# Optimization experiments

Hardware: AMD Instinct MI355X
Metric: run time of the kernel (lower is better)

Reference implementation:

```python
import jax, jax.numpy as jnp
import numpy as np

WH = WW = 7          # window size
N_TOK = WH * WW      # 49 tokens per window
HEADS = 8
HEAD_DIM = 32
DIM = HEADS * HEAD_DIM  # 256
NW = 64              # windows per image (56x56 / 7x7)
BW = 64 * NW         # batch_images * windows = 4096


def _rel_pos_index(wh, ww):
    # Swin-style relative position index, flattened to (N*N,)
    coords = np.stack(np.meshgrid(np.arange(wh), np.arange(ww), indexing='ij'))  # (2, wh, ww)
    coords = coords.reshape(2, -1)                                               # (2, N)
    rel = coords[:, :, None] - coords[:, None, :]                                # (2, N, N)
    rel = rel.transpose(1, 2, 0).astype(np.int64)                                # (N, N, 2)
    rel[:, :, 0] += wh - 1
    rel[:, :, 1] += ww - 1
    rel[:, :, 0] *= 2 * ww - 1
    return jnp.asarray(rel.sum(-1).reshape(-1))                                  # (N*N,)

_REL_IDX = _rel_pos_index(WH, WW)


def setup_inputs() -> dict:
    key = jax.random.key(0)
    ks = jax.random.split(key, 5)
    x = jax.random.normal(ks[0], (BW, N_TOK, DIM), dtype=jnp.float32)
    mask = jnp.zeros((1, NW, 1, N_TOK, N_TOK), dtype=jnp.float32)
    w_qkv = jax.random.normal(ks[1], (DIM, 3 * HEADS * HEAD_DIM), dtype=jnp.float32) * 0.02
    b_qkv = jnp.zeros((3 * HEADS * HEAD_DIM,), dtype=jnp.float32)
    rel_table = jax.random.normal(ks[2], ((2 * WH - 1) * (2 * WW - 1), HEADS), dtype=jnp.float32) * 0.02
    w_out = jax.random.normal(ks[3], (HEADS * HEAD_DIM, DIM), dtype=jnp.float32) * 0.02
    b_out = jnp.zeros((DIM,), dtype=jnp.float32)
    return {"x": x, "mask": mask, "w_qkv": w_qkv, "b_qkv": b_qkv,
            "rel_table": rel_table, "w_out": w_out, "b_out": b_out}


def reference(x, mask, w_qkv, b_qkv, rel_table, w_out, b_out):
    bw, n, d = x.shape
    # QKV projection then split per original Rearrange:
    # 'b n (qkv h hd) -> qkv b h n hd'
    qkv = (x @ w_qkv + b_qkv).reshape(bw, n, 3, HEADS, HEAD_DIM)
    qkv = qkv.transpose(2, 0, 3, 1, 4)  # (3, bw, h, n, hd)
    q, k, v = qkv[0], qkv[1], qkv[2]
    # NOTE: original computes einsum('bnid,bnjd->bnij', k, q): a[i,j] = k_i . q_j
    a = jnp.einsum('bhid,bhjd->bhij', k, q) / jnp.sqrt(jnp.asarray(HEAD_DIM, x.dtype))
    # relative position bias: table gather then '(i j) h -> h i j'
    bias = rel_table[_REL_IDX].reshape(n, n, HEADS).transpose(2, 0, 1)  # (h, n, n)
    a = a + bias
    # mask add: '(b nW) h i j -> b nW h i j', + mask, back
    nw = mask.shape[1]
    a = a.reshape(bw // nw, nw, HEADS, n, n) + mask
    a = a.reshape(bw, HEADS, n, n)
    a = jax.nn.softmax(a, axis=-1)
    y = jnp.einsum('bhij,bhjd->bhid', a, v)        # (bw, h, n, hd)
    y = y.transpose(0, 2, 1, 3).reshape(bw, n, HEADS * HEAD_DIM)
    return y @ w_out + b_out
```

## Files before the change

### kernel.cpp

```cpp
#include <hip/hip_runtime.h>

typedef __attribute__((ext_vector_type(8))) short short8;
typedef __attribute__((ext_vector_type(4))) float f32x4;
typedef unsigned short u16;

#define NTOK 49
#define NBLK 4096

#define XF  0
#define QKP 16384
#define VTF 49152
#define MKF 65536
#define BQ  73728
#define BO  75264
#define POOL 75776

#define WS_WQT 0
#define WS_WOT 393216
#define WS_BIAS 524288

__device__ __forceinline__ u16 f2bf(float f) {
  unsigned u = __float_as_uint(f);
  return (u16)((u + 0x7fffu + ((u >> 16) & 1u)) >> 16);
}
__device__ __forceinline__ unsigned packbf(float a, float b) {
  return (unsigned)f2bf(a) | ((unsigned)f2bf(b) << 16);
}

__global__ void prep_kernel(const float* __restrict__ w_qkv,
                            const float* __restrict__ w_out,
                            const float* __restrict__ rel,
                            u16* __restrict__ wqTf,
                            u16* __restrict__ woTf,
                            float* __restrict__ biasf) {
  const int stride = gridDim.x * blockDim.x;
  const int gid = blockIdx.x * blockDim.x + threadIdx.x;
  for (int e = gid; e < 48 * 8 * 64 * 8; e += stride) {
    int eL = e & 7, ln = (e >> 3) & 63, ks = (e >> 9) & 7, ctg = e >> 12;
    int k = ks * 32 + (ln >> 4) * 8 + eL;
    int c = ctg * 16 + (ln & 15);
    wqTf[e] = f2bf(w_qkv[k * 768 + c]);
  }
  for (int e = gid; e < 16 * 8 * 64 * 8; e += stride) {
    int eL = e & 7, ln = (e >> 3) & 63, ks = (e >> 9) & 7, ctg = e >> 12;
    int k = ks * 32 + (ln >> 4) * 8 + eL;
    int c = ctg * 16 + (ln & 15);
    woTf[e] = f2bf(w_out[k * 256 + c]);
  }
  for (int e = gid; e < 8 * 16 * 64 * 4; e += stride) {
    int rg = e & 3, ln = (e >> 2) & 63, t = (e >> 8) & 15, hh = e >> 12;
    int i = (t >> 2) * 16 + (ln & 15);
    int j = (t & 3) * 16 + (ln >> 4) * 4 + rg;
    float v;
    if (j >= NTOK) v = -1e30f;
    else if (i >= NTOK) v = 0.f;
    else {
      int dh = i / 7 - j / 7 + 6;
      int dw = i % 7 - j % 7 + 6;
      v = rel[(dh * 13 + dw) * 8 + hh];
    }
    biasf[e] = v;
  }
}

__global__ void __launch_bounds__(1024, 4) winattn_mfma(
    const float* __restrict__ x,
    const float* __restrict__ mask,
    const float* __restrict__ b_qkv,
    const float* __restrict__ b_out,
    const u16* __restrict__ wqTf,
    const u16* __restrict__ woTf,
    const float* __restrict__ biasf,
    float* __restrict__ out)
{
  __shared__ u16 pool[POOL];
  const int b = blockIdx.x, tid = threadIdx.x;
  const int lane = tid & 63, lo = lane & 15, hi = lane >> 4;
  const int w = tid >> 6;
  const int h = w & 7;
  const int it0 = (w >> 3) * 2;
  const f32x4 zf = {0.f, 0.f, 0.f, 0.f};
  float* mkf = (float*)(pool + MKF);
  float* bq  = (float*)(pool + BQ);
  float* bo  = (float*)(pool + BO);

  {
    const float4* xg = (const float4*)(x + (size_t)b * (NTOK * 256));
    for (int e = tid; e < 49 * 64; e += 1024) {
      float4 v = xg[e];
      int r = e >> 6, c4 = (e & 63) << 2;
      int addr = (((r >> 4) * 8 + (c4 >> 5)) * 64 + ((c4 >> 3) & 3) * 16 + (r & 15)) * 8 + (c4 & 7);
      *(uint2*)&pool[XF + addr] = make_uint2(packbf(v.x, v.y), packbf(v.z, v.w));
    }
    if (tid < 15 * 64) {
      int e = tid;
      int r = 49 + (e >> 6), c4 = (e & 63) << 2;
      int addr = (((r >> 4) * 8 + (c4 >> 5)) * 64 + ((c4 >> 3) & 3) * 16 + (r & 15)) * 8 + (c4 & 7);
      *(uint2*)&pool[XF + addr] = make_uint2(0u, 0u);
    }
    const float* mrow = mask + (size_t)(b & 63) * (NTOK * NTOK);
    for (int e = tid; e < 4096; e += 1024) {
      int rg = e & 3, l = (e >> 2) & 63, t = e >> 8;
      int i = (t >> 2) * 16 + (l & 15);
      int j = (t & 3) * 16 + (l >> 4) * 4 + rg;
      mkf[e] = (i < NTOK && j < NTOK) ? mrow[i * NTOK + j] : 0.f;
    }
    if (tid < 768) bq[tid] = b_qkv[tid];
    if (tid < 256) bo[tid] = b_out[tid];
  }
  __syncthreads();

  {
    f32x4 acc[3][4];
    #pragma unroll
    for (int ct = 0; ct < 3; ++ct)
      #pragma unroll
      for (int rt = 0; rt < 4; ++rt) acc[ct][rt] = zf;
    #pragma unroll
    for (int ks = 0; ks < 8; ++ks) {
      short8 bx[4];
      #pragma unroll
      for (int rt = 0; rt < 4; ++rt)
        bx[rt] = *(const short8*)&pool[XF + ((rt * 8 + ks) * 64 + lane) * 8];
      #pragma unroll
      for (int ct = 0; ct < 3; ++ct) {
        short8 af = *(const short8*)&wqTf[((size_t)((3 * w + ct) * 8 + ks) * 64 + lane) * 8];
        #pragma unroll
        for (int rt = 0; rt < 4; ++rt)
          acc[ct][rt] = __builtin_amdgcn_mfma_f32_16x16x32_bf16(af, bx[rt], acc[ct][rt], 0, 0, 0);
      }
    }
    #pragma unroll
    for (int ct = 0; ct < 3; ++ct) {
      const int ctg = 3 * w + ct;
      const int head2 = (ctg & 15) >> 1;
      f32x4 bias = *(const f32x4*)&bq[ctg * 16 + hi * 4];
      #pragma unroll
      for (int rt = 0; rt < 4; ++rt) {
        f32x4 v = acc[ct][rt] + bias;
        if (ctg < 32) {
          int base = QKP + head2 * 4096 + (ctg >= 16 ? 2048 : 0);
          int hi2 = (ctg & 1) * 2 + (hi >> 1);
          int eb = (hi & 1) * 4;
          *(uint2*)&pool[base + (rt * 64 + hi2 * 16 + lo) * 8 + eb] =
              make_uint2(packbf(v[0], v[1]), packbf(v[2], v[3]));
        } else {
          int dblk = ctg & 1;
          int ks2 = rt >> 1;
          int hi2 = (rt & 1) * 2 + (lo >> 3);
          int e2 = lo & 7;
          int vb = VTF + head2 * 2048 + ((dblk * 2 + ks2) * 64 + hi2 * 16) * 8 + e2;
          pool[vb + (hi * 4 + 0) * 8] = f2bf(v[0]);
          pool[vb + (hi * 4 + 1) * 8] = f2bf(v[1]);
          pool[vb + (hi * 4 + 2) * 8] = f2bf(v[2]);
          pool[vb + (hi * 4 + 3) * 8] = f2bf(v[3]);
        }
      }
    }
  }
  __syncthreads();

  float rs0 = 0.f, rs1 = 0.f;
  unsigned pkp[4][2][2];
  {
    short8 ka0 = *(const short8*)&pool[QKP + h * 4096 + 2048 + ((it0 + 0) * 64 + lane) * 8];
    short8 ka1 = *(const short8*)&pool[QKP + h * 4096 + 2048 + ((it0 + 1) * 64 + lane) * 8];
    const float* bh = biasf + ((size_t)h << 12);
    #pragma unroll
    for (int jt = 0; jt < 4; ++jt) {
      short8 qa = *(const short8*)&pool[QKP + h * 4096 + (jt * 64 + lane) * 8];
      f32x4 s0 = __builtin_amdgcn_mfma_f32_16x16x32_bf16(qa, ka0, zf, 0, 0, 0);
      f32x4 s1 = __builtin_amdgcn_mfma_f32_16x16x32_bf16(qa, ka1, zf, 0, 0, 0);
      {
        const int t = (it0 + 0) * 4 + jt;
        f32x4 bm = *(const f32x4*)&bh[(t * 64 + lane) * 4];
        f32x4 mm = *(const f32x4*)&mkf[(t * 64 + lane) * 4];
        float p0 = __expf(fmaf(s0[0], 0.17677669529663687f, bm[0] + mm[0]));
        float p1 = __expf(fmaf(s0[1], 0.17677669529663687f, bm[1] + mm[1]));
        float p2 = __expf(fmaf(s0[2], 0.17677669529663687f, bm[2] + mm[2]));
        float p3 = __expf(fmaf(s0[3], 0.17677669529663687f, bm[3] + mm[3]));
        rs0 += (p0 + p1) + (p2 + p3);
        pkp[jt][0][0] = packbf(p0, p1);
        pkp[jt][0][1] = packbf(p2, p3);
      }
      {
        const int t = (it0 + 1) * 4 + jt;
        f32x4 bm = *(const f32x4*)&bh[(t * 64 + lane) * 4];
        f32x4 mm = *(const f32x4*)&mkf[(t * 64 + lane) * 4];
        float p0 = __expf(fmaf(s1[0], 0.17677669529663687f, bm[0] + mm[0]));
        float p1 = __expf(fmaf(s1[1], 0.17677669529663687f, bm[1] + mm[1]));
        float p2 = __expf(fmaf(s1[2], 0.17677669529663687f, bm[2] + mm[2]));
        float p3 = __expf(fmaf(s1[3], 0.17677669529663687f, bm[3] + mm[3]));
        rs1 += (p0 + p1) + (p2 + p3);
        pkp[jt][1][0] = packbf(p0, p1);
        pkp[jt][1][1] = packbf(p2, p3);
      }
    }
  }
  float inv0, inv1;
  {
    float r2 = rs0 + __shfl_xor(rs0, 16);
    inv0 = 1.f / (r2 + __shfl_xor(r2, 32));
    float r3 = rs1 + __shfl_xor(rs1, 16);
    inv1 = 1.f / (r3 + __shfl_xor(r3, 32));
  }

  {
    short8 va[2][2];
    #pragma unroll
    for (int dblk = 0; dblk < 2; ++dblk)
      #pragma unroll
      for (int k2 = 0; k2 < 2; ++k2)
        va[dblk][k2] = *(const short8*)&pool[VTF + h * 2048 + ((dblk * 2 + k2) * 64 + lane) * 8];
    f32x4 ya[2][2];
    ya[0][0] = zf; ya[0][1] = zf; ya[1][0] = zf; ya[1][1] = zf;
    const int src0 = lo + ((hi & 1) * 2) * 16;
    const int src1 = src0 + 16;
    const bool hiSel = (hi & 2) != 0;
    #pragma unroll
    for (int itL = 0; itL < 2; ++itL)
      #pragma unroll
      for (int k2 = 0; k2 < 2; ++k2) {
        unsigned a0 = (unsigned)__shfl((int)pkp[2 * k2][itL][0], src0);
        unsigned b0 = (unsigned)__shfl((int)pkp[2 * k2 + 1][itL][0], src0);
        unsigned a1 = (unsigned)__shfl((int)pkp[2 * k2][itL][1], src0);
        unsigned b1 = (unsigned)__shfl((int)pkp[2 * k2 + 1][itL][1], src0);
        unsigned a2 = (unsigned)__shfl((int)pkp[2 * k2][itL][0], src1);
        unsigned b2 = (unsigned)__shfl((int)pkp[2 * k2 + 1][itL][0], src1);
        unsigned a3 = (unsigned)__shfl((int)pkp[2 * k2][itL][1], src1);
        unsigned b3 = (unsigned)__shfl((int)pkp[2 * k2 + 1][itL][1], src1);
        union { unsigned u[4]; short8 s8; } pb;
        pb.u[0] = hiSel ? b0 : a0;
        pb.u[1] = hiSel ? b1 : a1;
        pb.u[2] = hiSel ? b2 : a2;
        pb.u[3] = hiSel ? b3 : a3;
        ya[0][itL] = __builtin_amdgcn_mfma_f32_16x16x32_bf16(va[0][k2], pb.s8, ya[0][itL], 0, 0, 0);
        ya[1][itL] = __builtin_amdgcn_mfma_f32_16x16x32_bf16(va[1][k2], pb.s8, ya[1][itL], 0, 0, 0);
      }
    #pragma unroll
    for (int itL = 0; itL < 2; ++itL) {
      const float inv = itL ? inv1 : inv0;
      #pragma unroll
      for (int dblk = 0; dblk < 2; ++dblk) {
        float y0 = ya[dblk][itL][0] * inv;
        float y1 = ya[dblk][itL][1] * inv;
        float y2 = ya[dblk][itL][2] * inv;
        float y3 = ya[dblk][itL][3] * inv;
        int hi2 = dblk * 2 + (hi >> 1);
        int eb = (hi & 1) * 4;
        *(uint2*)&pool[XF + (((it0 + itL) * 8 + h) * 64 + hi2 * 16 + lo) * 8 + eb] =
            make_uint2(packbf(y0, y1), packbf(y2, y3));
      }
    }
  }
  __syncthreads();

  {
    f32x4 pacc[4];
    pacc[0] = zf; pacc[1] = zf; pacc[2] = zf; pacc[3] = zf;
    #pragma unroll
    for (int ks = 0; ks < 8; ++ks) {
      short8 wf = *(const short8*)&woTf[((size_t)(w * 8 + ks) * 64 + lane) * 8];
      #pragma unroll
      for (int rt = 0; rt < 4; ++rt) {
        short8 yb = *(const short8*)&pool[XF + ((rt * 8 + ks) * 64 + lane) * 8];
        pacc[rt] = __builtin_amdgcn_mfma_f32_16x16x32_bf16(wf, yb, pacc[rt], 0, 0, 0);
      }
    }
    float* og = out + (size_t)b * (NTOK * 256);
    const int cb = w * 16 + hi * 4;
    f32x4 bb = *(const f32x4*)&bo[cb];
    #pragma unroll
    for (int rt = 0; rt < 4; ++rt) {
      const int r = rt * 16 + lo;
      if (r < NTOK) {
        f32x4 vv = pacc[rt] + bb;
        *(f32x4*)(og + (size_t)r * 256 + cb) = vv;
      }
    }
  }
}

extern "C" void kernel_launch(void* const* d_in, const int* in_sizes, int n_in,
                              void* d_out, int out_size, void* d_ws, size_t ws_size,
                              hipStream_t stream) {
  const float *x = nullptr, *mask = nullptr, *w_qkv = nullptr, *b_qkv = nullptr,
              *rel_t = nullptr, *w_out = nullptr, *b_out = nullptr;
  for (int i = 0; i < n_in; ++i) {
    const float* p = (const float*)d_in[i];
    switch (in_sizes[i]) {
      case 4096 * 49 * 256: x = p; break;
      case 64 * 49 * 49:    mask = p; break;
      case 256 * 768:       w_qkv = p; break;
      case 768:             b_qkv = p; break;
      case 169 * 8:         rel_t = p; break;
      case 256 * 256:       w_out = p; break;
      case 256:             b_out = p; break;
    }
  }
  char* wsb = (char*)d_ws;
  u16* wqTf = (u16*)(wsb + WS_WQT);
  u16* woTf = (u16*)(wsb + WS_WOT);
  float* biasf = (float*)(wsb + WS_BIAS);

  hipLaunchKernelGGL(prep_kernel, dim3(512), dim3(256), 0, stream,
                     w_qkv, w_out, rel_t, wqTf, woTf, biasf);
  hipLaunchKernelGGL(winattn_mfma, dim3(NBLK), dim3(1024), 0, stream,
                     x, mask, b_qkv, b_out, wqTf, woTf, biasf, (float*)d_out);
}
```

Baseline: 290.0 us.

## Precompute mask in fragment layout, swizzle X in LDS, transpose V projection output

Moves the per-window mask reordering into the prep kernel as a global fragment-layout buffer pre-scaled by log2(e), so the main kernel no longer stages mask and biases in shared memory and shared memory shrinks from about 148KB to 128KB. The X tile in LDS gets an XOR swizzle meant to cut bank conflicts. Q/K/V column groups are reassigned per warp so the V projection uses swapped MFMA operands and stores packed 8-byte writes instead of scalar 2-byte stores. Softmax switches from exp to exp2 with the scale folded in. The mask and bias are now read from global memory on every block, which relies on L2 hits.

```diff
diff --git a/kernel.cpp b/kernel.cpp
--- a/kernel.cpp
+++ b/kernel.cpp
@@ -6,18 +6,17 @@
 
 #define NTOK 49
 #define NBLK 4096
+#define LOG2E 1.4426950408889634f
 
 #define XF  0
 #define QKP 16384
 #define VTF 49152
-#define MKF 65536
-#define BQ  73728
-#define BO  75264
-#define POOL 75776
+#define POOLN 65536
 
 #define WS_WQT 0
 #define WS_WOT 393216
 #define WS_BIAS 524288
+#define WS_MKG 655360
 
 __device__ __forceinline__ u16 f2bf(float f) {
   unsigned u = __float_as_uint(f);
@@ -27,12 +26,33 @@
   return (unsigned)f2bf(a) | ((unsigned)f2bf(b) << 16);
 }
 
+__device__ __forceinline__ short8 asm_frag(unsigned c0p0, unsigned c0p1,
+                                           unsigned c1p0, unsigned c1p1,
+                                           int srcA, int srcB, bool cSel) {
+  unsigned a0 = (unsigned)__shfl((int)c0p0, srcA);
+  unsigned b0 = (unsigned)__shfl((int)c1p0, srcA);
+  unsigned a1 = (unsigned)__shfl((int)c0p1, srcA);
+  unsigned b1 = (unsigned)__shfl((int)c1p1, srcA);
+  unsigned a2 = (unsigned)__shfl((int)c0p0, srcB);
+  unsigned b2 = (unsigned)__shfl((int)c1p0, srcB);
+  unsigned a3 = (unsigned)__shfl((int)c0p1, srcB);
+  unsigned b3 = (unsigned)__shfl((int)c1p1, srcB);
+  union { unsigned u[4]; short8 s8; } r;
+  r.u[0] = cSel ? b0 : a0;
+  r.u[1] = cSel ? b1 : a1;
+  r.u[2] = cSel ? b2 : a2;
+  r.u[3] = cSel ? b3 : a3;
+  return r.s8;
+}
+
 __global__ void prep_kernel(const float* __restrict__ w_qkv,
                             const float* __restrict__ w_out,
                             const float* __restrict__ rel,
+                            const float* __restrict__ mask,
                             u16* __restrict__ wqTf,
                             u16* __restrict__ woTf,
-                            float* __restrict__ biasf) {
+                            float* __restrict__ biasf,
+                            float* __restrict__ mkg) {
   const int stride = gridDim.x * blockDim.x;
   const int gid = blockIdx.x * blockDim.x + threadIdx.x;
   for (int e = gid; e < 48 * 8 * 64 * 8; e += stride) {
@@ -59,102 +79,103 @@
       int dw = i % 7 - j % 7 + 6;
       v = rel[(dh * 13 + dw) * 8 + hh];
     }
-    biasf[e] = v;
+    biasf[e] = v * LOG2E;
+  }
+  for (int e = gid; e < 64 * 16 * 64 * 4; e += stride) {
+    int rg = e & 3, ln = (e >> 2) & 63, t = (e >> 8) & 15, wdw = e >> 12;
+    int i = (t >> 2) * 16 + (ln & 15);
+    int j = (t & 3) * 16 + (ln >> 4) * 4 + rg;
+    mkg[e] = (i < NTOK && j < NTOK) ? mask[wdw * (NTOK * NTOK) + i * NTOK + j] * LOG2E : 0.f;
   }
 }
 
 __global__ void __launch_bounds__(1024, 4) winattn_mfma(
     const float* __restrict__ x,
-    const float* __restrict__ mask,
     const float* __restrict__ b_qkv,
     const float* __restrict__ b_out,
     const u16* __restrict__ wqTf,
     const u16* __restrict__ woTf,
     const float* __restrict__ biasf,
+    const float* __restrict__ mkg,
     float* __restrict__ out)
 {
-  __shared__ u16 pool[POOL];
+  __shared__ u16 pool[POOLN];
   const int b = blockIdx.x, tid = threadIdx.x;
   const int lane = tid & 63, lo = lane & 15, hi = lane >> 4;
   const int w = tid >> 6;
   const int h = w & 7;
   const int it0 = (w >> 3) * 2;
   const f32x4 zf = {0.f, 0.f, 0.f, 0.f};
-  float* mkf = (float*)(pool + MKF);
-  float* bq  = (float*)(pool + BQ);
-  float* bo  = (float*)(pool + BO);
 
   {
     const float4* xg = (const float4*)(x + (size_t)b * (NTOK * 256));
     for (int e = tid; e < 49 * 64; e += 1024) {
       float4 v = xg[e];
-      int r = e >> 6, c4 = (e & 63) << 2;
-      int addr = (((r >> 4) * 8 + (c4 >> 5)) * 64 + ((c4 >> 3) & 3) * 16 + (r & 15)) * 8 + (c4 & 7);
-      *(uint2*)&pool[XF + addr] = make_uint2(packbf(v.x, v.y), packbf(v.z, v.w));
+      int r = e >> 6, ks = (e >> 3) & 7, sub = (e >> 1) & 3, eb = (e & 1) * 4;
+      int unit = ((r >> 4) * 8 + ks) * 64 + sub * 16 + ((r & 15) ^ ((2 * sub + ks) & 15));
+      *(uint2*)&pool[XF + unit * 8 + eb] = make_uint2(packbf(v.x, v.y), packbf(v.z, v.w));
     }
     if (tid < 15 * 64) {
       int e = tid;
-      int r = 49 + (e >> 6), c4 = (e & 63) << 2;
-      int addr = (((r >> 4) * 8 + (c4 >> 5)) * 64 + ((c4 >> 3) & 3) * 16 + (r & 15)) * 8 + (c4 & 7);
-      *(uint2*)&pool[XF + addr] = make_uint2(0u, 0u);
-    }
-    const float* mrow = mask + (size_t)(b & 63) * (NTOK * NTOK);
-    for (int e = tid; e < 4096; e += 1024) {
-      int rg = e & 3, l = (e >> 2) & 63, t = e >> 8;
-      int i = (t >> 2) * 16 + (l & 15);
-      int j = (t & 3) * 16 + (l >> 4) * 4 + rg;
-      mkf[e] = (i < NTOK && j < NTOK) ? mrow[i * NTOK + j] : 0.f;
-    }
-    if (tid < 768) bq[tid] = b_qkv[tid];
-    if (tid < 256) bo[tid] = b_out[tid];
+      int r = 49 + (e >> 6), c = e & 63;
+      int ks = c >> 3, sub = (c >> 1) & 3, eb = (c & 1) * 4;
+      int unit = ((r >> 4) * 8 + ks) * 64 + sub * 16 + ((r & 15) ^ ((2 * sub + ks) & 15));
+      *(uint2*)&pool[XF + unit * 8 + eb] = make_uint2(0u, 0u);
+    }
   }
   __syncthreads();
 
   {
+    const int ctq0 = 2 * w, ctq1 = 2 * w + 1, ctv = 32 + w;
     f32x4 acc[3][4];
     #pragma unroll
     for (int ct = 0; ct < 3; ++ct)
       #pragma unroll
       for (int rt = 0; rt < 4; ++rt) acc[ct][rt] = zf;
+    const int lo2 = 2 * hi;
     #pragma unroll
     for (int ks = 0; ks < 8; ++ks) {
+      const int swz = (lo ^ ((lo2 + ks) & 15));
       short8 bx[4];
       #pragma unroll
       for (int rt = 0; rt < 4; ++rt)
-        bx[rt] = *(const short8*)&pool[XF + ((rt * 8 + ks) * 64 + lane) * 8];
-      #pragma unroll
-      for (int ct = 0; ct < 3; ++ct) {
-        short8 af = *(const short8*)&wqTf[((size_t)((3 * w + ct) * 8 + ks) * 64 + lane) * 8];
-        #pragma unroll
-        for (int rt = 0; rt < 4; ++rt)
-          acc[ct][rt] = __builtin_amdgcn_mfma_f32_16x16x32_bf16(af, bx[rt], acc[ct][rt], 0, 0, 0);
-      }
-    }
-    #pragma unroll
-    for (int ct = 0; ct < 3; ++ct) {
-      const int ctg = 3 * w + ct;
-      const int head2 = (ctg & 15) >> 1;
-      f32x4 bias = *(const f32x4*)&bq[ctg * 16 + hi * 4];
+        bx[rt] = *(const short8*)&pool[XF + (((rt * 8 + ks) * 64) + hi * 16 + swz) * 8];
+      short8 af0 = *(const short8*)&wqTf[((size_t)(ctq0 * 8 + ks) * 64 + lane) * 8];
+      short8 af1 = *(const short8*)&wqTf[((size_t)(ctq1 * 8 + ks) * 64 + lane) * 8];
+      short8 afv = *(const short8*)&wqTf[((size_t)(ctv * 8 + ks) * 64 + lane) * 8];
+      #pragma unroll
+      for (int rt = 0; rt < 4; ++rt) {
+        acc[0][rt] = __builtin_amdgcn_mfma_f32_16x16x32_bf16(af0, bx[rt], acc[0][rt], 0, 0, 0);
+        acc[1][rt] = __builtin_amdgcn_mfma_f32_16x16x32_bf16(af1, bx[rt], acc[1][rt], 0, 0, 0);
+        acc[2][rt] = __builtin_amdgcn_mfma_f32_16x16x32_bf16(bx[rt], afv, acc[2][rt], 0, 0, 0);
+      }
+    }
+    const int qkbase = QKP + (w & 7) * 4096 + ((w >= 8) ? 2048 : 0);
+    #pragma unroll
+    for (int ct = 0; ct < 2; ++ct) {
+      const int ctg = 2 * w + ct;
+      f32x4 bias = *(const f32x4*)(b_qkv + ctg * 16 + hi * 4);
       #pragma unroll
       for (int rt = 0; rt < 4; ++rt) {
         f32x4 v = acc[ct][rt] + bias;
-        if (ctg < 32) {
-          int base = QKP + head2 * 4096 + (ctg >= 16 ? 2048 : 0);
-          int hi2 = (ctg & 1) * 2 + (hi >> 1);
-          int eb = (hi & 1) * 4;
-          *(uint2*)&pool[base + (rt * 64 + hi2 * 16 + lo) * 8 + eb] =
-              make_uint2(packbf(v[0], v[1]), packbf(v[2], v[3]));
-        } else {
-          int dblk = ctg & 1;
-          int ks2 = rt >> 1;
-          int hi2 = (rt & 1) * 2 + (lo >> 3);
-          int e2 = lo & 7;
-          int vb = VTF + head2 * 2048 + ((dblk * 2 + ks2) * 64 + hi2 * 16) * 8 + e2;
-          pool[vb + (hi * 4 + 0) * 8] = f2bf(v[0]);
-          pool[vb + (hi * 4 + 1) * 8] = f2bf(v[1]);
-          pool[vb + (hi * 4 + 2) * 8] = f2bf(v[2]);
-          pool[vb + (hi * 4 + 3) * 8] = f2bf(v[3]);
-        }
+        int hi2 = ct * 2 + (hi >> 1);
+        int eb = (hi & 1) * 4;
+        *(uint2*)&pool[qkbase + (rt * 64 + hi2 * 16 + lo) * 8 + eb] =
+            make_uint2(packbf(v[0], v[1]), packbf(v[2], v[3]));
+      }
+    }
+    {
+      const int vhead = w >> 1, dblk = w & 1;
+      const float bv = b_qkv[ctv * 16 + lo];
+      #pragma unroll
+      for (int rt = 0; rt < 4; ++rt) {
+        f32x4 v = acc[2][rt];
+        float v0 = v[0] + bv, v1 = v[1] + bv, v2 = v[2] + bv, v3 = v[3] + bv;
+        int f = dblk * 2 + (rt >> 1);
+        int hiR = (rt & 1) * 2 + (hi >> 1);
+        int eb = (hi & 1) * 4;
+        *(uint2*)&pool[VTF + (f * 8 + vhead) * 512 + (hiR * 16 + lo) * 8 + eb] =
+            make_uint2(packbf(v0, v1), packbf(v2, v3));
       }
     }
   }
@@ -163,9 +184,11 @@
   float rs0 = 0.f, rs1 = 0.f;
   unsigned pkp[4][2][2];
   {
+    const float SC = 0.17677669529663687f * LOG2E;
     short8 ka0 = *(const short8*)&pool[QKP + h * 4096 + 2048 + ((it0 + 0) * 64 + lane) * 8];
     short8 ka1 = *(const short8*)&pool[QKP + h * 4096 + 2048 + ((it0 + 1) * 64 + lane) * 8];
-    const float* bh = biasf + ((size_t)h << 12);
+    const float* bh = biasf + h * 4096;
+    const float* mh = mkg + (size_t)(b & 63) * 4096;
     #pragma unroll
     for (int jt = 0; jt < 4; ++jt) {
       short8 qa = *(const short8*)&pool[QKP + h * 4096 + (jt * 64 + lane) * 8];
@@ -174,11 +197,11 @@
       {
         const int t = (it0 + 0) * 4 + jt;
         f32x4 bm = *(const f32x4*)&bh[(t * 64 + lane) * 4];
-        f32x4 mm = *(const f32x4*)&mkf[(t * 64 + lane) * 4];
-        float p0 = __expf(fmaf(s0[0], 0.17677669529663687f, bm[0] + mm[0]));
-        float p1 = __expf(fmaf(s0[1], 0.17677669529663687f, bm[1] + mm[1]));
-        float p2 = __expf(fmaf(s0[2], 0.17677669529663687f, bm[2] + mm[2]));
-        float p3 = __expf(fmaf(s0[3], 0.17677669529663687f, bm[3] + mm[3]));
+        f32x4 mm = *(const f32x4*)&mh[(t * 64 + lane) * 4];
+        float p0 = exp2f(fmaf(s0[0], SC, bm[0] + mm[0]));
+        float p1 = exp2f(fmaf(s0[1], SC, bm[1] + mm[1]));
+        float p2 = exp2f(fmaf(s0[2], SC, bm[2] + mm[2]));
+        float p3 = exp2f(fmaf(s0[3], SC, bm[3] + mm[3]));
         rs0 += (p0 + p1) + (p2 + p3);
         pkp[jt][0][0] = packbf(p0, p1);
         pkp[jt][0][1] = packbf(p2, p3);
@@ -186,11 +209,11 @@
       {
         const int t = (it0 + 1) * 4 + jt;
         f32x4 bm = *(const f32x4*)&bh[(t * 64 + lane) * 4];
-        f32x4 mm = *(const f32x4*)&mkf[(t * 64 + lane) * 4];
-        float p0 = __expf(fmaf(s1[0], 0.17677669529663687f, bm[0] + mm[0]));
-        float p1 = __expf(fmaf(s1[1], 0.17677669529663687f, bm[1] + mm[1]));
-        float p2 = __expf(fmaf(s1[2], 0.17677669529663687f, bm[2] + mm[2]));
-        float p3 = __expf(fmaf(s1[3], 0.17677669529663687f, bm[3] + mm[3]));
+        f32x4 mm = *(const f32x4*)&mh[(t * 64 + lane) * 4];
+        float p0 = exp2f(fmaf(s1[0], SC, bm[0] + mm[0]));
+        float p1 = exp2f(fmaf(s1[1], SC, bm[1] + mm[1]));
+        float p2 = exp2f(fmaf(s1[2], SC, bm[2] + mm[2]));
+        float p3 = exp2f(fmaf(s1[3], SC, bm[3] + mm[3]));
         rs1 += (p0 + p1) + (p2 + p3);
         pkp[jt][1][0] = packbf(p0, p1);
         pkp[jt][1][1] = packbf(p2, p3);
@@ -206,50 +229,36 @@
   }
 
   {
+    const int srcA = lo + 32 * (hi & 1);
+    const int srcB = srcA + 16;
+    const bool cSel = (hi & 2) != 0;
     short8 va[2][2];
     #pragma unroll
     for (int dblk = 0; dblk < 2; ++dblk)
       #pragma unroll
       for (int k2 = 0; k2 < 2; ++k2)
-        va[dblk][k2] = *(const short8*)&pool[VTF + h * 2048 + ((dblk * 2 + k2) * 64 + lane) * 8];
+        va[dblk][k2] = *(const short8*)&pool[VTF + ((dblk * 2 + k2) * 8 + h) * 512 + lane * 8];
     f32x4 ya[2][2];
     ya[0][0] = zf; ya[0][1] = zf; ya[1][0] = zf; ya[1][1] = zf;
-    const int src0 = lo + ((hi & 1) * 2) * 16;
-    const int src1 = src0 + 16;
-    const bool hiSel = (hi & 2) != 0;
     #pragma unroll
     for (int itL = 0; itL < 2; ++itL)
       #pragma unroll
       for (int k2 = 0; k2 < 2; ++k2) {
-        unsigned a0 = (unsigned)__shfl((int)pkp[2 * k2][itL][0], src0);
-        unsigned b0 = (unsigned)__shfl((int)pkp[2 * k2 + 1][itL][0], src0);
-        unsigned a1 = (unsigned)__shfl((int)pkp[2 * k2][itL][1], src0);
-        unsigned b1 = (unsigned)__shfl((int)pkp[2 * k2 + 1][itL][1], src0);
-        unsigned a2 = (unsigned)__shfl((int)pkp[2 * k2][itL][0], src1);
-        unsigned b2 = (unsigned)__shfl((int)pkp[2 * k2 + 1][itL][0], src1);
-        unsigned a3 = (unsigned)__shfl((int)pkp[2 * k2][itL][1], src1);
-        unsigned b3 = (unsigned)__shfl((int)pkp[2 * k2 + 1][itL][1], src1);
-        union { unsigned u[4]; short8 s8; } pb;
-        pb.u[0] = hiSel ? b0 : a0;
-        pb.u[1] = hiSel ? b1 : a1;
-        pb.u[2] = hiSel ? b2 : a2;
-        pb.u[3] = hiSel ? b3 : a3;
-        ya[0][itL] = __builtin_amdgcn_mfma_f32_16x16x32_bf16(va[0][k2], pb.s8, ya[0][itL], 0, 0, 0);
-        ya[1][itL] = __builtin_amdgcn_mfma_f32_16x16x32_bf16(va[1][k2], pb.s8, ya[1][itL], 0, 0, 0);
+        short8 pb = asm_frag(pkp[2 * k2][itL][0], pkp[2 * k2][itL][1],
+                             pkp[2 * k2 + 1][itL][0], pkp[2 * k2 + 1][itL][1], srcA, srcB, cSel);
+        ya[0][itL] = __builtin_amdgcn_mfma_f32_16x16x32_bf16(va[0][k2], pb, ya[0][itL], 0, 0, 0);
+        ya[1][itL] = __builtin_amdgcn_mfma_f32_16x16x32_bf16(va[1][k2], pb, ya[1][itL], 0, 0, 0);
       }
     #pragma unroll
     for (int itL = 0; itL < 2; ++itL) {
-      const float inv = itL ? inv1 : inv0;
+      const float iv = itL ? inv1 : inv0;
       #pragma unroll
       for (int dblk = 0; dblk < 2; ++dblk) {
-        float y0 = ya[dblk][itL][0] * inv;
-        float y1 = ya[dblk][itL][1] * inv;
-        float y2 = ya[dblk][itL][2] * inv;
-        float y3 = ya[dblk][itL][3] * inv;
+        f32x4 yy = ya[dblk][itL];
         int hi2 = dblk * 2 + (hi >> 1);
         int eb = (hi & 1) * 4;
         *(uint2*)&pool[XF + (((it0 + itL) * 8 + h) * 64 + hi2 * 16 + lo) * 8 + eb] =
-            make_uint2(packbf(y0, y1), packbf(y2, y3));
+            make_uint2(packbf(yy[0] * iv, yy[1] * iv), packbf(yy[2] * iv, yy[3] * iv));
       }
     }
   }
@@ -269,7 +278,7 @@
     }
     float* og = out + (size_t)b * (NTOK * 256);
     const int cb = w * 16 + hi * 4;
-    f32x4 bb = *(const f32x4*)&bo[cb];
+    f32x4 bb = *(const f32x4*)(b_out + cb);
     #pragma unroll
     for (int rt = 0; rt < 4; ++rt) {
       const int r = rt * 16 + lo;
@@ -299,12 +308,13 @@
     }
   }
   char* wsb = (char*)d_ws;
-  u16* wqTf = (u16*)(wsb + WS_WQT);
-  u16* woTf = (u16*)(wsb + WS_WOT);
+  u16* wqTf    = (u16*)(wsb + WS_WQT);
+  u16* woTf    = (u16*)(wsb + WS_WOT);
   float* biasf = (float*)(wsb + WS_BIAS);
-
-  hipLaunchKernelGGL(prep_kernel, dim3(512), dim3(256), 0, stream,
-                     w_qkv, w_out, rel_t, wqTf, woTf, biasf);
+  float* mkg   = (float*)(wsb + WS_MKG);
+
+  hipLaunchKernelGGL(prep_kernel, dim3(1024), dim3(256), 0, stream,
+                     w_qkv, w_out, rel_t, mask, wqTf, woTf, biasf, mkg);
   hipLaunchKernelGGL(winattn_mfma, dim3(NBLK), dim3(1024), 0, stream,
-                     x, mask, b_qkv, b_out, wqTf, woTf, biasf, (float*)d_out);
-}
+                     x, b_qkv, b_out, wqTf, woTf, biasf, mkg, (float*)d_out);
+}
```

After: 318.9 us. 1.1x slower.
